# Performance work log

Hardware: AMD Instinct MI355X
Metric: run time of the kernel (lower is better)

Reference implementation:

```python
import jax, jax.numpy as jnp
import numpy as np
from jax import lax

TEMPERATURE = 0.0005


def conv1d(x, w, b, pad):
    # x: [B, Cin, T], w: [Cout, Cin, K], b: [Cout]
    y = lax.conv_general_dilated(x, w, window_strides=(1,), padding=[(pad, pad)],
                                 dimension_numbers=('NCH', 'OIH', 'NCH'))
    return y + b[None, :, None]


def setup_inputs() -> dict:
    key = jax.random.key(0)
    ks = jax.random.split(key, 16)
    B, Cq, Ck, Ca, Tde, Ten = 32, 80, 512, 80, 2000, 400

    def xavier(k, shape):
        fan_in = shape[1] * (shape[2] if len(shape) > 2 else 1)
        fan_out = shape[0] * (shape[2] if len(shape) > 2 else 1)
        lim = float(np.sqrt(6.0 / (fan_in + fan_out)))
        return jax.random.uniform(k, shape, jnp.float32, -lim, lim)

    inp = {
        'queries': jax.random.normal(ks[0], (B, Cq, Tde), jnp.float32),
        'keys': jax.random.normal(ks[1], (B, Ck, Ten), jnp.float32),
        'mask': jnp.ones((B, 1, Ten), jnp.int32),
        # key_layer: Conv(512->1024,k3,p1) -> ReLU -> Conv(1024->80,k1)
        'kw1': xavier(ks[2], (Ck * 2, Ck, 3)), 'kb1': jnp.zeros((Ck * 2,), jnp.float32),
        'kw2': xavier(ks[3], (Ca, Ck * 2, 1)), 'kb2': jnp.zeros((Ca,), jnp.float32),
        # query_layer: Conv(80->160,k3,p1)->ReLU->Conv(160->80,k1)->ReLU->Conv(80->80,k1)
        'qw1': xavier(ks[4], (Cq * 2, Cq, 3)), 'qb1': jnp.zeros((Cq * 2,), jnp.float32),
        'qw2': xavier(ks[5], (Cq, Cq * 2, 1)), 'qb2': jnp.zeros((Cq,), jnp.float32),
        'qw3': xavier(ks[6], (Ca, Cq, 1)), 'qb3': jnp.zeros((Ca,), jnp.float32),
    }
    return inp


def reference(queries, keys, mask, kw1, kb1, kw2, kb2, qw1, qb1, qw2, qb2, qw3, qb3):
    # key path: conv3 -> relu -> conv1
    k = conv1d(jax.nn.relu(conv1d(keys, kw1, kb1, 1)), kw2, kb2, 0)          # [B,Ca,Ten]
    # query path: conv3 -> relu -> conv1 -> relu -> conv1
    q = conv1d(queries, qw1, qb1, 1)
    q = jax.nn.relu(conv1d(jax.nn.relu(q), qw2, qb2, 0))
    q = conv1d(q, qw3, qb3, 0)                                               # [B,Ca,Tde]

    # sum_c (q - k)^2 = |q|^2 + |k|^2 - 2 q.k  (avoids [B,C,Tde,Ten] intermediate)
    q2 = jnp.sum(q * q, axis=1)                      # [B,Tde]
    k2 = jnp.sum(k * k, axis=1)                      # [B,Ten]
    qk = jnp.einsum('bcd,bce->bde', q, k)            # [B,Tde,Ten]
    dist = q2[:, :, None] + k2[:, None, :] - 2.0 * qk
    attn_logp = (-TEMPERATURE * dist)[:, None]       # [B,1,Tde,Ten]

    # masked fill over encoder positions (softmax dim)
    m = mask.astype(bool)[:, :, None, :]             # [B,1,1,Ten]
    attn_logp = jnp.where(m, attn_logp, -jnp.inf)
    attn = jax.nn.softmax(attn_logp, axis=3)
    return attn, attn_logp
```

## Files before the change

kernel.cpp:

```cpp
#include <hip/hip_runtime.h>
#include <hip/hip_bf16.h>
#include <math.h>

#define NB 32
#define CK 512
#define C1 1024
#define CA 80
#define CQ 80
#define CQ2 160
#define TEN 400
#define TDE 2000
#define KDIM 1536
#define TPAD 448
#define TQP 2048

static constexpr float TEMP = 0.0005f;

typedef __attribute__((ext_vector_type(8))) short short8;
typedef __attribute__((ext_vector_type(4))) float f32x4;

__device__ inline short f2bf(float v) {
  __hip_bfloat16 h = __float2bfloat16(v);
  return *(short*)&h;
}
__device__ inline float bf2f(short s) {
  __hip_bfloat16 h = *(__hip_bfloat16*)&s;
  return __bfloat162float(h);
}

__device__ inline void gload_lds16(const void* g, void* l) {
  __builtin_amdgcn_global_load_lds(
      (const __attribute__((address_space(1))) unsigned int*)g,
      (__attribute__((address_space(3))) unsigned int*)l, 16, 0, 0);
}

__global__ __launch_bounds__(256) void cvt_weights_kernel(
    const float* __restrict__ kw1, const float* __restrict__ kw2,
    const float* __restrict__ qw1, const float* __restrict__ qw2,
    const float* __restrict__ qw3, short* __restrict__ w1bf,
    short* __restrict__ w2bf, short* __restrict__ w1q,
    short* __restrict__ w2q, short* __restrict__ w3q) {
  int i = blockIdx.x * 256 + threadIdx.x;
  if (i < 1572864) {
    w1bf[i] = f2bf(kw1[i]);
    return;
  }
  i -= 1572864;
  if (i < 131072) {
    int r = i >> 10, c = i & 1023;
    w2bf[i] = f2bf(r < CA ? kw2[r * 1024 + c] : 0.f);
    return;
  }
  i -= 131072;
  if (i < 49152) {
    int r = i >> 8, c = i & 255;
    w1q[i] = f2bf((r < CQ2 && c < 240) ? qw1[r * 240 + c] : 0.f);
    return;
  }
  i -= 49152;
  if (i < 20480) {
    int r = i / 160, c = i - r * 160;
    w2q[i] = f2bf(r < CA ? qw2[r * 160 + c] : 0.f);
    return;
  }
  i -= 20480;
  if (i < 12288) {
    int r = i / 96, c = i - r * 96;
    w3q[i] = f2bf((r < CA && c < CQ) ? qw3[r * 80 + c] : 0.f);
  }
}

__global__ __launch_bounds__(256) void im2col_kernel(
    const float* __restrict__ keys, short* __restrict__ BmatT) {
  const int t = blockIdx.x;
  const int b = blockIdx.y;
  const int tid = threadIdx.x;
  short* dst = BmatT + ((size_t)b * TPAD + t) * KDIM;
  #pragma unroll
  for (int i = 0; i < 6; ++i) {
    int k = tid + i * 256;
    int ci = k / 3;
    int dk = k - ci * 3;
    int ts = t + dk - 1;
    float v = (ts >= 0 && ts < TEN) ? keys[((size_t)b * CK + ci) * TEN + ts] : 0.f;
    dst[k] = f2bf(v);
  }
}

__global__ __launch_bounds__(256) void im2col_q_kernel(
    const float* __restrict__ queries, short* __restrict__ Bq) {
  const int t = blockIdx.x;
  const int b = blockIdx.y;
  const int k = threadIdx.x;
  float v = 0.f;
  if (t < TDE && k < 240) {
    int ci = k / 3, dk = k - ci * 3, ts = t + dk - 1;
    v = (ts >= 0 && ts < TDE) ? queries[((size_t)b * CQ + ci) * TDE + ts] : 0.f;
  }
  Bq[((size_t)b * TQP + t) * 256 + k] = f2bf(v);
}

__global__ __launch_bounds__(256) void kconv1_mfma_kernel(
    const short* __restrict__ w1bf, const short* __restrict__ BmatT,
    const float* __restrict__ b1, short* __restrict__ k1t) {
  __shared__ short A_lds[4096];
  __shared__ short B_lds[4096];
  const int flat = blockIdx.x;
  const int cox = flat >> 7;
  const int rem = flat & 127;
  const int b   = rem >> 2;
  const int ty  = rem & 3;
  const int co0 = cox * 128;
  const int t0  = ty * 128;
  const int tid = threadIdx.x;
  const int l = tid & 63, w = tid >> 6;

  auto invswz = [](int Y) {
    int X = Y;
    X ^= ((Y >> 8) & 1) << 6;
    X ^= ((Y >> 7) & 1) << 5;
    X ^= (((Y >> 6) ^ (Y >> 8)) & 1) << 4;
    return X;
  };

  const short* gsrc[4];
  short* ldst[4];
  #pragma unroll
  for (int j = 0; j < 4; ++j) {
    int c = w * 4 + j;
    int Y = (c & 7) * 1024 + l * 16;
    int X = invswz(Y);
    int row = X >> 6, slot = (X >> 4) & 3;
    if (c < 8) {
      gsrc[j] = w1bf + (size_t)(co0 + row) * KDIM + slot * 8;
      ldst[j] = &A_lds[(c & 7) * 512];
    } else {
      int gr = t0 + row;
      if (gr > TPAD - 1) gr = TPAD - 1;
      gsrc[j] = BmatT + ((size_t)b * TPAD + gr) * KDIM + slot * 8;
      ldst[j] = &B_lds[(c & 7) * 512];
    }
  }

  const int kslot = l >> 4;
  int abyte[2];
  #pragma unroll
  for (int i = 0; i < 2; ++i) {
    int arow = w * 32 + i * 16 + (l & 15);
    abyte[i] = (arow * 64 + kslot * 16) ^ ((arow & 7) << 4);
  }
  int bbyte[8];
  #pragma unroll
  for (int g = 0; g < 8; ++g) {
    int brow = g * 16 + (l & 15);
    bbyte[g] = (brow * 64 + kslot * 16) ^ ((brow & 7) << 4);
  }

  f32x4 acc[2][8];
  #pragma unroll
  for (int i = 0; i < 2; ++i)
    #pragma unroll
    for (int g = 0; g < 8; ++g) acc[i][g] = (f32x4){0.f, 0.f, 0.f, 0.f};

  for (int kt = 0; kt < KDIM / 32; ++kt) {
    __syncthreads();
    #pragma unroll
    for (int j = 0; j < 4; ++j) gload_lds16(gsrc[j] + kt * 32, ldst[j]);
    __syncthreads();
    short8 a0 = *(const short8*)((const char*)A_lds + abyte[0]);
    short8 a1 = *(const short8*)((const char*)A_lds + abyte[1]);
    #pragma unroll
    for (int g = 0; g < 8; ++g) {
      short8 bb = *(const short8*)((const char*)B_lds + bbyte[g]);
      acc[0][g] = __builtin_amdgcn_mfma_f32_16x16x32_bf16(a0, bb, acc[0][g], 0, 0, 0);
      acc[1][g] = __builtin_amdgcn_mfma_f32_16x16x32_bf16(a1, bb, acc[1][g], 0, 0, 0);
    }
  }

  #pragma unroll
  for (int g = 0; g < 8; ++g) {
    int t = t0 + g * 16 + (l & 15);
    if (t < TEN) {
      #pragma unroll
      for (int i = 0; i < 2; ++i) {
        #pragma unroll
        for (int r = 0; r < 4; ++r) {
          int co = co0 + w * 32 + i * 16 + kslot * 4 + r;
          float v = acc[i][g][r] + b1[co];
          k1t[((size_t)b * TPAD + t) * C1 + co] = f2bf(v > 0.f ? v : 0.f);
        }
      }
    }
  }
}

template <int MODE, bool RELU>
__global__ __launch_bounds__(256) void qgemm_kernel(
    const short* __restrict__ A, const short* __restrict__ B,
    const float* __restrict__ bias, void* __restrict__ outv,
    int M, int Kpad, int kiters, int Nvalid, int outCols,
    size_t bBatchStride, size_t outBatchStride, int outLD) {
  __shared__ short A_lds[2048];
  __shared__ short B_lds[2048];
  const int co0 = blockIdx.x * 64;
  const int t0  = blockIdx.y * 64;
  const int b   = blockIdx.z;
  const int tid = threadIdx.x;
  const int l = tid & 63, w = tid >> 6;
  const int srow = tid >> 2, sslot = tid & 3;

  const short* gA = A + (size_t)(co0 + srow) * Kpad + sslot * 8;
  const short* gB = B + (size_t)b * bBatchStride + (size_t)(t0 + srow) * Kpad + sslot * 8;
  const int wbyte = (srow * 64 + sslot * 16) ^ ((srow & 7) << 4);

  const int kslot = l >> 4;
  const int arow = w * 16 + (l & 15);
  const int abyte = (arow * 64 + kslot * 16) ^ ((arow & 7) << 4);
  int bbyte[4];
  #pragma unroll
  for (int g = 0; g < 4; ++g) {
    int brow = g * 16 + (l & 15);
    bbyte[g] = (brow * 64 + kslot * 16) ^ ((brow & 7) << 4);
  }

  f32x4 acc[4];
  #pragma unroll
  for (int g = 0; g < 4; ++g) acc[g] = (f32x4){0.f, 0.f, 0.f, 0.f};

  uint4 av = *(const uint4*)gA;
  uint4 bv = *(const uint4*)gB;
  for (int kt = 0; kt < kiters; ++kt) {
    __syncthreads();
    *(uint4*)((char*)A_lds + wbyte) = av;
    *(uint4*)((char*)B_lds + wbyte) = bv;
    __syncthreads();
    uint4 an = av, bn = bv;
    if (kt + 1 < kiters) {
      an = *(const uint4*)(gA + (kt + 1) * 32);
      bn = *(const uint4*)(gB + (kt + 1) * 32);
    }
    short8 a = *(const short8*)((const char*)A_lds + abyte);
    #pragma unroll
    for (int g = 0; g < 4; ++g) {
      short8 bb = *(const short8*)((const char*)B_lds + bbyte[g]);
      acc[g] = __builtin_amdgcn_mfma_f32_16x16x32_bf16(a, bb, acc[g], 0, 0, 0);
    }
    av = an; bv = bn;
  }

  #pragma unroll
  for (int g = 0; g < 4; ++g) {
    int t = t0 + g * 16 + (l & 15);
    if (t >= Nvalid) continue;
    #pragma unroll
    for (int r = 0; r < 4; ++r) {
      int co = co0 + w * 16 + kslot * 4 + r;
      if (MODE == 1) {
        if (co < outCols) {
          float v = 0.f;
          if (co < M) {
            v = acc[g][r] + bias[co];
            if (RELU) v = v > 0.f ? v : 0.f;
          }
          ((short*)outv)[(size_t)b * outBatchStride + (size_t)t * outLD + co] = f2bf(v);
        }
      } else {
        if (co < M) {
          float v = acc[g][r] + bias[co];
          if (RELU) v = v > 0.f ? v : 0.f;
          ((float*)outv)[(size_t)b * outBatchStride + (size_t)co * outLD + t] = v;
        }
      }
    }
  }
}

__global__ __launch_bounds__(256) void norms_kernel(
    const short* __restrict__ qA, const short* __restrict__ kB,
    float* __restrict__ q2n, float* __restrict__ k2n) {
  const int tid = threadIdx.x;
  const int R = blockIdx.x * 64 + (tid >> 2);
  const int g = tid & 3;
  const short* src;
  float* dst;
  if (R < NB * TQP) {
    src = qA + (size_t)R * 96 + g * 24;
    dst = q2n + R;
  } else {
    int R2 = R - NB * TQP;
    if (R2 >= NB * TPAD) return;
    src = kB + (size_t)R2 * 96 + g * 24;
    dst = k2n + R2;
  }
  float s = 0.f;
  #pragma unroll
  for (int c = 0; c < 3; ++c) {
    short8 v = *(const short8*)(src + c * 8);
    #pragma unroll
    for (int j = 0; j < 8; ++j) {
      float f = bf2f(v[j]);
      s += f * f;
    }
  }
  s += __shfl_xor(s, 1, 64);
  s += __shfl_xor(s, 2, 64);
  if (g == 0) *dst = s;
}

__global__ __launch_bounds__(256) void attn_fused_kernel(
    const short* __restrict__ qA, const short* __restrict__ kB,
    const float* __restrict__ q2, const float* __restrict__ k2,
    const int* __restrict__ mask, float* __restrict__ out_attn,
    float* __restrict__ out_logp) {
  __shared__ short A_lds[3][2048];
  __shared__ short B_lds[3][2560];
  __shared__ float k2LDS[400];
  __shared__ int mLDS[400];
  const int t0 = blockIdx.x * 64;
  const int b  = blockIdx.y;
  const int tid = threadIdx.x;
  const int l = tid & 63, w = tid >> 6;

  {
    const int arow_s = tid >> 2, aslot = tid & 3;
    const short* gA = qA + ((size_t)b * TQP + t0 + arow_s) * 96 + aslot * 8;
    #pragma unroll
    for (int p = 0; p < 3; ++p) {
      uint4 v = *(const uint4*)(gA + p * 32);
      *(uint4*)((char*)&A_lds[p][0] +
                ((arow_s * 64 + aslot * 16) ^ ((arow_s & 7) << 4))) = v;
    }
  }
  for (int idx = tid; idx < 400; idx += 256) {
    k2LDS[idx] = k2[(size_t)b * TPAD + idx];
    mLDS[idx] = mask[(size_t)b * TEN + idx];
  }

  const int kslot = l >> 4;
  const int arow = w * 16 + (l & 15);
  const int abyte = (arow * 64 + kslot * 16) ^ ((arow & 7) << 4);

  f32x4 acc[25];
  #pragma unroll
  for (int i = 0; i < 25; ++i) acc[i] = (f32x4){0.f, 0.f, 0.f, 0.f};

  __syncthreads();
  #pragma unroll
  for (int st = 0; st < 5; ++st) {
    for (int idx = tid; idx < 960; idx += 256) {
      int row = idx / 12, c = idx - row * 12;
      int panel = c >> 2, ps = c & 3;
      uint4 v = *(const uint4*)(kB + ((size_t)b * TPAD + st * 80 + row) * 96 + c * 8);
      *(uint4*)((char*)&B_lds[panel][0] +
                ((row * 64 + ps * 16) ^ ((row & 7) << 4))) = v;
    }
    __syncthreads();
    #pragma unroll
    for (int kt = 0; kt < 3; ++kt) {
      short8 a = *(const short8*)((const char*)&A_lds[kt][0] + abyte);
      #pragma unroll
      for (int f = 0; f < 5; ++f) {
        int brow = f * 16 + (l & 15);
        short8 bb = *(const short8*)((const char*)&B_lds[kt][0] +
                                     ((brow * 64 + kslot * 16) ^ ((brow & 7) << 4)));
        acc[st * 5 + f] =
            __builtin_amdgcn_mfma_f32_16x16x32_bf16(a, bb, acc[st * 5 + f], 0, 0, 0);
      }
    }
    __syncthreads();
  }

  int trow[4]; float q2v[4];
  #pragma unroll
  for (int r = 0; r < 4; ++r) {
    trow[r] = t0 + w * 16 + kslot * 4 + r;
    q2v[r] = q2[(size_t)b * TQP + trow[r]];
  }
  #pragma unroll
  for (int sf = 0; sf < 25; ++sf) {
    int s = sf * 16 + (l & 15);
    float k2v = k2LDS[s];
    bool mk = mLDS[s] != 0;
    #pragma unroll
    for (int r = 0; r < 4; ++r) {
      float lp = mk ? (-TEMP) * (q2v[r] + k2v - 2.f * acc[sf][r]) : -INFINITY;
      acc[sf][r] = lp;
    }
  }
  #pragma unroll
  for (int r = 0; r < 4; ++r) {
    if (trow[r] < TDE) {
      float* dst = out_logp + ((size_t)(b * TDE + trow[r])) * TEN + (l & 15);
      #pragma unroll
      for (int sf = 0; sf < 25; ++sf) dst[sf * 16] = acc[sf][r];
    }
  }
  float m[4];
  #pragma unroll
  for (int r = 0; r < 4; ++r) m[r] = -INFINITY;
  #pragma unroll
  for (int sf = 0; sf < 25; ++sf)
    #pragma unroll
    for (int r = 0; r < 4; ++r) m[r] = fmaxf(m[r], acc[sf][r]);
  #pragma unroll
  for (int o = 1; o < 16; o <<= 1)
    #pragma unroll
    for (int r = 0; r < 4; ++r) m[r] = fmaxf(m[r], __shfl_xor(m[r], o, 64));
  float sum[4] = {0.f, 0.f, 0.f, 0.f};
  #pragma unroll
  for (int sf = 0; sf < 25; ++sf)
    #pragma unroll
    for (int r = 0; r < 4; ++r) {
      float v = acc[sf][r];
      float e = (v != -INFINITY) ? __expf(v - m[r]) : 0.f;
      acc[sf][r] = e;
      sum[r] += e;
    }
  #pragma unroll
  for (int o = 1; o < 16; o <<= 1)
    #pragma unroll
    for (int r = 0; r < 4; ++r) sum[r] += __shfl_xor(sum[r], o, 64);
  float inv[4];
  #pragma unroll
  for (int r = 0; r < 4; ++r) inv[r] = 1.0f / sum[r];
  #pragma unroll
  for (int r = 0; r < 4; ++r) {
    if (trow[r] < TDE) {
      float* dst = out_attn + ((size_t)(b * TDE + trow[r])) * TEN + (l & 15);
      #pragma unroll
      for (int sf = 0; sf < 25; ++sf) dst[sf * 16] = acc[sf][r] * inv[r];
    }
  }
}

extern "C" void kernel_launch(void* const* d_in, const int* in_sizes, int n_in,
                              void* d_out, int out_size, void* d_ws, size_t ws_size,
                              hipStream_t stream) {
  const float* queries = (const float*)d_in[0];
  const float* keys    = (const float*)d_in[1];
  const int*   mask    = (const int*)d_in[2];
  const float* kw1 = (const float*)d_in[3];
  const float* kb1 = (const float*)d_in[4];
  const float* kw2 = (const float*)d_in[5];
  const float* kb2 = (const float*)d_in[6];
  const float* qw1 = (const float*)d_in[7];
  const float* qb1 = (const float*)d_in[8];
  const float* qw2 = (const float*)d_in[9];
  const float* qb2 = (const float*)d_in[10];
  const float* qw3 = (const float*)d_in[11];
  const float* qb3 = (const float*)d_in[12];
  float* out = (float*)d_out;

  char* ws = (char*)d_ws;
  short* BmatT = (short*)ws;
  short* w1bf  = (short*)(ws + 44040192);
  short* k1t   = (short*)(ws + 47185920);
  short* w2bf  = (short*)(ws + 76546048);
  short* w1q   = (short*)(ws + 76808192);
  short* w2q   = (short*)(ws + 76906496);
  short* w3q   = (short*)(ws + 76947456);
  short* Bq    = (short*)ws;
  short* q1bf  = (short*)(ws + 33554432);
  short* q2bf  = (short*)(ws + 54525952);
  short* qA    = (short*)(ws + 20480000);
  float* q2n   = (float*)(ws + 33062912);
  float* k2n   = (float*)(ws + 49938432);
  short* kB    = (short*)(ws + 81920000);

  const long long HALF = 25600000LL;
  float* out_attn = out;
  float* out_logp = out + HALF;

  cvt_weights_kernel<<<dim3(6976), dim3(256), 0, stream>>>(
      kw1, kw2, qw1, qw2, qw3, w1bf, w2bf, w1q, w2q, w3q);

  im2col_kernel<<<dim3(TEN, NB), dim3(256), 0, stream>>>(keys, BmatT);
  kconv1_mfma_kernel<<<dim3(1024), dim3(256), 0, stream>>>(w1bf, BmatT, kb1, k1t);
  qgemm_kernel<1, false><<<dim3(2, 7, NB), dim3(256), 0, stream>>>(
      w2bf, k1t, kb2, kB, CA, C1, 32, TEN, 96,
      (size_t)TPAD * C1, (size_t)TPAD * 96, 96);

  im2col_q_kernel<<<dim3(TQP, NB), dim3(256), 0, stream>>>(queries, Bq);
  qgemm_kernel<1, true><<<dim3(3, TQP / 64, NB), dim3(256), 0, stream>>>(
      w1q, Bq, qb1, q1bf, CQ2, 256, 8, TQP, 160,
      (size_t)TQP * 256, (size_t)TQP * 160, 160);
  qgemm_kernel<1, true><<<dim3(2, TQP / 64, NB), dim3(256), 0, stream>>>(
      w2q, q1bf, qb2, q2bf, CA, 160, 5, TQP, 96,
      (size_t)TQP * 160, (size_t)TQP * 96, 96);
  qgemm_kernel<1, false><<<dim3(2, TQP / 64, NB), dim3(256), 0, stream>>>(
      w3q, q2bf, qb3, qA, CA, 96, 3, TQP, 96,
      (size_t)TQP * 96, (size_t)TQP * 96, 96);

  norms_kernel<<<dim3((NB * TQP + NB * TPAD) / 64), dim3(256), 0, stream>>>(
      qA, kB, q2n, k2n);
  attn_fused_kernel<<<dim3(TQP / 64, NB), dim3(256), 0, stream>>>(
      qA, kB, q2n, k2n, mask, out_attn, out_logp);
}
```

Before: 344.8 us.

## Replace im2col with padded transposed keys and per-tap shifted GEMM loop

Drops the explicit im2col buffer (3x expanded keys) for the key conv and instead writes a bf16 transposed, zero-padded copy of keys once. The conv GEMM loops over the three kernel taps and reads shifted rows of that copy, with the weights reordered tap-major to match. This cuts im2col write and read traffic and one pass of global memory. The trade-off is a transpose kernel with a low block count and slightly more address setup per tap.

```diff
diff --git a/kernel.cpp b/kernel.cpp
--- a/kernel.cpp
+++ b/kernel.cpp
@@ -10,9 +10,9 @@
 #define CQ2 160
 #define TEN 400
 #define TDE 2000
-#define KDIM 1536
 #define TPAD 448
 #define TQP 2048
+#define KTROWS 520
 
 static constexpr float TEMP = 0.0005f;
 
@@ -37,12 +37,14 @@
 __global__ __launch_bounds__(256) void cvt_weights_kernel(
     const float* __restrict__ kw1, const float* __restrict__ kw2,
     const float* __restrict__ qw1, const float* __restrict__ qw2,
-    const float* __restrict__ qw3, short* __restrict__ w1bf,
+    const float* __restrict__ qw3, short* __restrict__ w1p,
     short* __restrict__ w2bf, short* __restrict__ w1q,
     short* __restrict__ w2q, short* __restrict__ w3q) {
   int i = blockIdx.x * 256 + threadIdx.x;
   if (i < 1572864) {
-    w1bf[i] = f2bf(kw1[i]);
+    int co = i / 1536, rem = i - co * 1536;
+    int ci = rem / 3, dk = rem - ci * 3;
+    w1p[dk * 524288 + co * 512 + ci] = f2bf(kw1[i]);
     return;
   }
   i -= 1572864;
@@ -70,20 +72,26 @@
   }
 }
 
-__global__ __launch_bounds__(256) void im2col_kernel(
-    const float* __restrict__ keys, short* __restrict__ BmatT) {
-  const int t = blockIdx.x;
+__global__ __launch_bounds__(256) void transpose_keys_kernel(
+    const float* __restrict__ keys, short* __restrict__ keysT) {
+  __shared__ float sm[64][65];
+  const int rt = blockIdx.x * 64;
   const int b = blockIdx.y;
   const int tid = threadIdx.x;
-  short* dst = BmatT + ((size_t)b * TPAD + t) * KDIM;
-  #pragma unroll
-  for (int i = 0; i < 6; ++i) {
-    int k = tid + i * 256;
-    int ci = k / 3;
-    int dk = k - ci * 3;
-    int ts = t + dk - 1;
-    float v = (ts >= 0 && ts < TEN) ? keys[((size_t)b * CK + ci) * TEN + ts] : 0.f;
-    dst[k] = f2bf(v);
+  const int lane = tid & 63, quad = tid >> 6;
+  for (int ci0 = 0; ci0 < 512; ci0 += 64) {
+    for (int cc = quad; cc < 64; cc += 4) {
+      int t = rt + lane - 1;
+      sm[cc][lane] = (t >= 0 && t < TEN)
+                         ? keys[((size_t)b * CK + ci0 + cc) * TEN + t] : 0.f;
+    }
+    __syncthreads();
+    for (int jj = quad; jj < 64; jj += 4) {
+      int r = rt + jj;
+      if (r < KTROWS)
+        keysT[((size_t)b * KTROWS + r) * 512 + ci0 + lane] = f2bf(sm[lane][jj]);
+    }
+    __syncthreads();
   }
 }
 
@@ -101,7 +109,7 @@
 }
 
 __global__ __launch_bounds__(256) void kconv1_mfma_kernel(
-    const short* __restrict__ w1bf, const short* __restrict__ BmatT,
+    const short* __restrict__ w1p, const short* __restrict__ keysT,
     const float* __restrict__ b1, short* __restrict__ k1t) {
   __shared__ short A_lds[4096];
   __shared__ short B_lds[4096];
@@ -123,23 +131,18 @@
     return X;
   };
 
-  const short* gsrc[4];
+  int srow_[4], sslot_[4];
+  bool isA_[4];
   short* ldst[4];
   #pragma unroll
   for (int j = 0; j < 4; ++j) {
     int c = w * 4 + j;
     int Y = (c & 7) * 1024 + l * 16;
     int X = invswz(Y);
-    int row = X >> 6, slot = (X >> 4) & 3;
-    if (c < 8) {
-      gsrc[j] = w1bf + (size_t)(co0 + row) * KDIM + slot * 8;
-      ldst[j] = &A_lds[(c & 7) * 512];
-    } else {
-      int gr = t0 + row;
-      if (gr > TPAD - 1) gr = TPAD - 1;
-      gsrc[j] = BmatT + ((size_t)b * TPAD + gr) * KDIM + slot * 8;
-      ldst[j] = &B_lds[(c & 7) * 512];
-    }
+    srow_[j] = X >> 6;
+    sslot_[j] = (X >> 4) & 3;
+    isA_[j] = (c < 8);
+    ldst[j] = isA_[j] ? &A_lds[(c & 7) * 512] : &B_lds[(c & 7) * 512];
   }
 
   const int kslot = l >> 4;
@@ -162,18 +165,29 @@
     #pragma unroll
     for (int g = 0; g < 8; ++g) acc[i][g] = (f32x4){0.f, 0.f, 0.f, 0.f};
 
-  for (int kt = 0; kt < KDIM / 32; ++kt) {
-    __syncthreads();
-    #pragma unroll
-    for (int j = 0; j < 4; ++j) gload_lds16(gsrc[j] + kt * 32, ldst[j]);
-    __syncthreads();
-    short8 a0 = *(const short8*)((const char*)A_lds + abyte[0]);
-    short8 a1 = *(const short8*)((const char*)A_lds + abyte[1]);
-    #pragma unroll
-    for (int g = 0; g < 8; ++g) {
-      short8 bb = *(const short8*)((const char*)B_lds + bbyte[g]);
-      acc[0][g] = __builtin_amdgcn_mfma_f32_16x16x32_bf16(a0, bb, acc[0][g], 0, 0, 0);
-      acc[1][g] = __builtin_amdgcn_mfma_f32_16x16x32_bf16(a1, bb, acc[1][g], 0, 0, 0);
+  for (int dk = 0; dk < 3; ++dk) {
+    const short* gsrc[4];
+    #pragma unroll
+    for (int j = 0; j < 4; ++j) {
+      if (isA_[j])
+        gsrc[j] = w1p + dk * 524288 + (co0 + srow_[j]) * 512 + sslot_[j] * 8;
+      else
+        gsrc[j] = keysT + ((size_t)b * KTROWS + t0 + srow_[j] + dk) * 512 +
+                  sslot_[j] * 8;
+    }
+    for (int kt = 0; kt < 16; ++kt) {
+      __syncthreads();
+      #pragma unroll
+      for (int j = 0; j < 4; ++j) gload_lds16(gsrc[j] + kt * 32, ldst[j]);
+      __syncthreads();
+      short8 a0 = *(const short8*)((const char*)A_lds + abyte[0]);
+      short8 a1 = *(const short8*)((const char*)A_lds + abyte[1]);
+      #pragma unroll
+      for (int g = 0; g < 8; ++g) {
+        short8 bb = *(const short8*)((const char*)B_lds + bbyte[g]);
+        acc[0][g] = __builtin_amdgcn_mfma_f32_16x16x32_bf16(a0, bb, acc[0][g], 0, 0, 0);
+        acc[1][g] = __builtin_amdgcn_mfma_f32_16x16x32_bf16(a1, bb, acc[1][g], 0, 0, 0);
+      }
     }
   }
 
@@ -452,8 +466,8 @@
   float* out = (float*)d_out;
 
   char* ws = (char*)d_ws;
-  short* BmatT = (short*)ws;
-  short* w1bf  = (short*)(ws + 44040192);
+  short* keysT = (short*)ws;
+  short* w1p   = (short*)(ws + 44040192);
   short* k1t   = (short*)(ws + 47185920);
   short* w2bf  = (short*)(ws + 76546048);
   short* w1q   = (short*)(ws + 76808192);
@@ -472,10 +486,10 @@
   float* out_logp = out + HALF;
 
   cvt_weights_kernel<<<dim3(6976), dim3(256), 0, stream>>>(
-      kw1, kw2, qw1, qw2, qw3, w1bf, w2bf, w1q, w2q, w3q);
-
-  im2col_kernel<<<dim3(TEN, NB), dim3(256), 0, stream>>>(keys, BmatT);
-  kconv1_mfma_kernel<<<dim3(1024), dim3(256), 0, stream>>>(w1bf, BmatT, kb1, k1t);
+      kw1, kw2, qw1, qw2, qw3, w1p, w2bf, w1q, w2q, w3q);
+
+  transpose_keys_kernel<<<dim3(9, NB), dim3(256), 0, stream>>>(keys, keysT);
+  kconv1_mfma_kernel<<<dim3(1024), dim3(256), 0, stream>>>(w1p, keysT, kb1, k1t);
   qgemm_kernel<1, false><<<dim3(2, 7, NB), dim3(256), 0, stream>>>(
       w2bf, k1t, kb2, kB, CA, C1, 32, TEN, 96,
       (size_t)TPAD * C1, (size_t)TPAD * 96, 96);
```

New measurement: 362.1 us. +5.0%, slower.
